# Optimization experiments

Measured on AMD Instinct MI355X. Metric: run time of the kernel, lower is better.

Reference implementation:

```python
import jax, jax.numpy as jnp
import numpy as np

H, W = 256, 256
N = 512
BG = jnp.zeros(3, dtype=jnp.float32)  # background_color=(0,0,0)


def setup_inputs() -> dict:
    key = jax.random.key(0)
    k1, k2, k3, k4, k5 = jax.random.split(key, 5)
    # positions: xy in [-1.5,1.5], z in [2,6] so every gaussian passes the z>0.01 test
    xy = jax.random.uniform(k1, (N, 2), minval=-1.5, maxval=1.5, dtype=jnp.float32)
    zpos = jax.random.uniform(k2, (N, 1), minval=2.0, maxval=6.0, dtype=jnp.float32)
    positions = jnp.concatenate([xy, zpos], axis=-1)
    # PSD 3D covariances with ~0.05 world-space std
    A = 0.05 * jax.random.normal(k3, (N, 3, 3), dtype=jnp.float32)
    cov3d = A @ jnp.swapaxes(A, -1, -2) + 1e-6 * jnp.eye(3, dtype=jnp.float32)
    opacities = jax.random.uniform(k4, (N, 1), dtype=jnp.float32)
    colors = jax.random.uniform(k5, (N, 3), dtype=jnp.float32)
    K = jnp.array([[300.0, 0.0, 128.0], [0.0, 300.0, 128.0], [0.0, 0.0, 1.0]], dtype=jnp.float32)
    R = jnp.eye(3, dtype=jnp.float32)
    t = jnp.zeros(3, dtype=jnp.float32)
    return {"positions": positions, "cov3d": cov3d, "opacities": opacities,
            "colors": colors, "K": K, "R": R, "t": t}


def _render(positions, cov3d, opacities, colors, K, R, t):
    # --- project means to camera / image space ---
    means_cam = positions @ R.T + t                       # (N,3)
    z = means_cam[:, 2]                                   # all > 0.01 by construction
    proj = means_cam @ K.T                                # (N,3)
    means_2d = proj[:, :2] / proj[:, 2:3]                 # (N,2) pixel coords (x,y)

    # --- project 3D covariance to 2D: cov2d = J (R cov3d R^T) J^T + 0.3 I ---
    fx, fy = K[0, 0], K[1, 1]
    xc, yc = means_cam[:, 0], means_cam[:, 1]
    zero = jnp.zeros_like(z)
    J = jnp.stack([
        jnp.stack([fx / z, zero, -fx * xc / z**2], axis=-1),
        jnp.stack([zero, fy / z, -fy * yc / z**2], axis=-1),
    ], axis=1)                                            # (N,2,3)
    cov_cam = jnp.einsum('ij,njk,lk->nil', R, cov3d, R)   # (N,3,3)
    cov2d = jnp.einsum('nij,njk,nlk->nil', J, cov_cam, J) + 0.3 * jnp.eye(2, dtype=jnp.float32)

    # --- front-to-back depth sort ---
    order = jnp.argsort(z)
    means_2d = means_2d[order]
    cov2d = cov2d[order]
    opac = opacities[:, 0][order]
    cols = colors[order]

    # --- 2x2 inverse and 3-sigma radii ---
    a, b, c = cov2d[:, 0, 0], cov2d[:, 0, 1], cov2d[:, 1, 1]
    det = jnp.clip(a * c - b * b, 1e-8, None)
    inv00, inv01, inv11 = c / det, -b / det, a / det
    max_eig = (a + c) * 0.5 + jnp.sqrt(jnp.clip(((a - c) * 0.5) ** 2 + b ** 2, 1e-8, None))
    radii = 3.0 * jnp.sqrt(max_eig)

    # --- bounding boxes (int() truncates toward zero, as in torch) ---
    mx, my = means_2d[:, 0], means_2d[:, 1]
    x_min = jnp.maximum(0.0, jnp.trunc(mx - radii))
    x_max = jnp.minimum(float(W), jnp.trunc(mx + radii) + 1.0)
    y_min = jnp.maximum(0.0, jnp.trunc(my - radii))
    y_max = jnp.minimum(float(H), jnp.trunc(my + radii) + 1.0)

    xs = jnp.arange(W, dtype=jnp.float32)
    ys = jnp.arange(H, dtype=jnp.float32)
    dx = xs[None, :] - mx[:, None]                        # (N,W)
    dy = ys[None, :] - my[:, None]                        # (N,H)
    mask_x = (xs[None, :] >= x_min[:, None]) & (xs[None, :] < x_max[:, None])
    mask_y = (ys[None, :] >= y_min[:, None]) & (ys[None, :] < y_max[:, None])
    mask = (mask_y[:, :, None] & mask_x[:, None, :]).astype(jnp.float32)  # (N,H,W)

    # --- gaussian weights on the grid ---
    mahal = (inv00[:, None, None] * dx[:, None, :] ** 2
             + 2.0 * inv01[:, None, None] * dy[:, :, None] * dx[:, None, :]
             + inv11[:, None, None] * dy[:, :, None] ** 2)                 # (N,H,W)
    alpha = opac[:, None, None] * jnp.exp(-0.5 * mahal) * mask            # (N,H,W)

    # --- front-to-back alpha compositing ---
    # sequential: contrib_i = alpha_i * (1 - alpha_acc_{i-1}); alpha_acc_i += contrib_i
    # closed form: T_i = prod_{j<i} (1 - alpha_j)  (exclusive cumprod)
    T = jnp.concatenate([jnp.ones((1, H, W), dtype=alpha.dtype),
                         jnp.cumprod(1.0 - alpha, axis=0)[:-1]], axis=0)
    contrib = alpha * T                                                   # (N,H,W)
    image = BG[None, None, :] + jnp.einsum('nhw,nc->hwc', contrib, cols)  # (H,W,3)
    return image


def reference(positions, cov3d, opacities, colors, K, R, t):
    return _render(positions, cov3d, opacities, colors, K, R, t)
```

## Files before the change

kernel.cpp:

```cpp
#include <hip/hip_runtime.h>


constexpr int IMG_H = 256;
constexpr int IMG_W = 256;
constexpr int MAXN  = 512;
constexpr int TW    = 16;
constexpr int TH    = 16;
constexpr int NTHR  = 512;

__global__ __launch_bounds__(NTHR) void fused_raster_kernel(
    const float* __restrict__ positions,
    const float* __restrict__ cov3d,
    const float* __restrict__ opacities,
    const float* __restrict__ colors,
    const float* __restrict__ Km,
    const float* __restrict__ Rm,
    const float* __restrict__ tv,
    float* __restrict__ out)
{
    __shared__ float4 s_srt[(MAXN + 4) * 3];
    __shared__ unsigned long long s_key[MAXN];
    __shared__ float4 s_comb[TW * TH];
    __shared__ int s_total;

    const int tix  = threadIdx.x;
    const int ty   = threadIdx.y;
    const int tid  = ty * TW + tix;
    const int lane = tid & 63;
    const int half = ty >> 4;
    const int py   = ty & 15;

    if (tid == 0) s_total = 0;

    const int tx0i = blockIdx.x * TW;
    const int ty0i = blockIdx.y * TH;
    const float tx0 = (float)tx0i;
    const float ty0 = (float)ty0i;

    const float R00 = Rm[0], R01 = Rm[1], R02 = Rm[2];
    const float R10 = Rm[3], R11 = Rm[4], R12 = Rm[5];
    const float R20 = Rm[6], R21 = Rm[7], R22 = Rm[8];
    const float t0 = tv[0], t1 = tv[1], t2 = tv[2];
    const float K00 = Km[0], K01 = Km[1], K02 = Km[2];
    const float K10 = Km[3], K11 = Km[4], K12 = Km[5];
    const float K20 = Km[6], K21 = Km[7], K22 = Km[8];
    const float fx = K00, fy = K11;

    __syncthreads();

    const int g = tid;

    const float px = positions[g*3+0];
    const float py3 = positions[g*3+1];
    const float pz = positions[g*3+2];

    const float cx = R00*px + R01*py3 + R02*pz + t0;
    const float cy = R10*px + R11*py3 + R12*pz + t1;
    const float cz = R20*px + R21*py3 + R22*pz + t2;

    const float pr0 = K00*cx + K01*cy + K02*cz;
    const float pr1 = K10*cx + K11*cy + K12*cz;
    const float pr2 = K20*cx + K21*cy + K22*cz;
    const float mx = pr0 / pr2;
    const float my = pr1 / pr2;

    const float invz  = 1.0f / cz;
    const float invz2 = invz * invz;
    const float j00 =  fx * invz;
    const float j02 = -fx * cx * invz2;
    const float j11 =  fy * invz;
    const float j12 = -fy * cy * invz2;

    const float C00 = cov3d[g*9+0], C01 = cov3d[g*9+1], C02 = cov3d[g*9+2];
    const float C10 = cov3d[g*9+3], C11 = cov3d[g*9+4], C12 = cov3d[g*9+5];
    const float C20 = cov3d[g*9+6], C21 = cov3d[g*9+7], C22 = cov3d[g*9+8];

    const float T100 = R00*C00 + R01*C10 + R02*C20;
    const float T101 = R00*C01 + R01*C11 + R02*C21;
    const float T102 = R00*C02 + R01*C12 + R02*C22;
    const float T110 = R10*C00 + R11*C10 + R12*C20;
    const float T111 = R10*C01 + R11*C11 + R12*C21;
    const float T112 = R10*C02 + R11*C12 + R12*C22;
    const float T120 = R20*C00 + R21*C10 + R22*C20;
    const float T121 = R20*C01 + R21*C11 + R22*C21;
    const float T122 = R20*C02 + R21*C12 + R22*C22;
    const float M00 = T100*R00 + T101*R01 + T102*R02;
    const float M01 = T100*R10 + T101*R11 + T102*R12;
    const float M02 = T100*R20 + T101*R21 + T102*R22;
    const float M11 = T110*R10 + T111*R11 + T112*R12;
    const float M12 = T110*R20 + T111*R21 + T112*R22;
    const float M20 = T120*R00 + T121*R01 + T122*R02;
    const float M21 = T120*R10 + T121*R11 + T122*R12;
    const float M22 = T120*R20 + T121*R21 + T122*R22;

    const float v00 = M00*j00 + M02*j02;
    const float v02 = M20*j00 + M22*j02;
    const float v10 = M01*j11 + M02*j12;
    const float v11 = M11*j11 + M12*j12;
    const float v12 = M21*j11 + M22*j12;

    const float va = j00*v00 + j02*v02 + 0.3f;
    const float vb = j00*v10 + j02*v12;
    const float vc = j11*v11 + j12*v12 + 0.3f;

    const float det  = fmaxf(va*vc - vb*vb, 1e-8f);
    const float idet = 1.0f / det;
    const float inv00 =  vc * idet;
    const float inv01 = -vb * idet;
    const float inv11 =  va * idet;

    const float half_diff = (va - vc) * 0.5f;
    const float disc = fmaxf(half_diff*half_diff + vb*vb, 1e-8f);
    const float max_eig = (va + vc) * 0.5f + sqrtf(disc);
    const float radii = 3.0f * sqrtf(max_eig);

    const float x_min = fmaxf(0.0f, truncf(mx - radii));
    const float x_max = fminf((float)IMG_W, truncf(mx + radii) + 1.0f);
    const float y_min = fmaxf(0.0f, truncf(my - radii));
    const float y_max = fminf((float)IMG_H, truncf(my + radii) + 1.0f);

    const unsigned long long key =
        ((unsigned long long)__float_as_uint(cz) << 32) | (unsigned)g;

    const bool hit = (x_min < tx0 + (float)TW) && (x_max > tx0) &&
                     (y_min < ty0 + (float)TH) && (y_max > ty0);

    {
        const unsigned long long mb = __ballot(hit);
        int base = 0;
        if (lane == 0 && mb) base = atomicAdd(&s_total, __popcll(mb));
        base = __shfl(base, 0);
        if (hit) {
            const int pos = base + __popcll(mb & ((1ull << lane) - 1ull));
            s_key[pos] = key;
        }
    }
    __syncthreads();
    const int K = s_total;

    int rank = 0;
    for (int j = 0; j < K; ++j)
        rank += (s_key[j] < key) ? 1 : 0;

    if (hit) {
        const int xm = max(0,  (int)x_min - tx0i);
        const int xM = min(TW, (int)x_max - tx0i);
        const int ym = max(0,  (int)y_min - ty0i);
        const int yM = min(TH, (int)y_max - ty0i);
        const unsigned pk = (unsigned)xm | ((unsigned)xM << 5)
                          | ((unsigned)ym << 10) | ((unsigned)yM << 15);
        s_srt[rank*3+0] = make_float4(mx, my, -0.5f*inv00, -inv01);
        s_srt[rank*3+1] = make_float4(-0.5f*inv11, opacities[g],
                                      colors[g*3+0], colors[g*3+1]);
        s_srt[rank*3+2] = make_float4(colors[g*3+2], __uint_as_float(pk),
                                      0.0f, 0.0f);
    }
    if (tid < 6) s_srt[K*3 + tid] = make_float4(0.0f, 0.0f, 0.0f, 0.0f);
    __syncthreads();

    int Kf = (K + 1) >> 1;
    Kf += (Kf & 1);
    if (Kf > K) Kf = K + (K & 1);
    const int mStart = half ? Kf : 0;
    const int mEnd   = half ? K  : Kf;

    const float fxp = (float)(tx0i + tix);
    const float fyp = (float)(ty0i + py);

    float T = 1.0f, accr = 0.0f, accg = 0.0f, accb = 0.0f;

    const int sb = mStart * 3;
    float4 A0 = s_srt[sb+0], A1 = s_srt[sb+1], A2 = s_srt[sb+2];
    float4 B0 = s_srt[sb+3], B1 = s_srt[sb+4], B2 = s_srt[sb+5];

    for (int m = mStart; m < mEnd; m += 2) {
        const int pf = (m + 2) * 3;
        const float4 C0 = s_srt[pf+0], C1 = s_srt[pf+1], C2 = s_srt[pf+2];
        const float4 D0 = s_srt[pf+3], D1 = s_srt[pf+4], D2 = s_srt[pf+5];

        {
            const unsigned pk = __float_as_uint(A2.y);
            const bool in = (tix >= (int)(pk & 31u)) & (tix < (int)((pk >> 5) & 31u))
                          & (py >= (int)((pk >> 10) & 31u)) & (py < (int)((pk >> 15) & 31u));
            const float dx = fxp - A0.x;
            const float dy = fyp - A0.y;
            const float e = A0.z*dx*dx + A0.w*dx*dy + A1.x*dy*dy;
            const float a = in ? A1.y * __expf(e) : 0.0f;
            const float w = T * a;
            accr = fmaf(w, A1.z, accr);
            accg = fmaf(w, A1.w, accg);
            accb = fmaf(w, A2.x, accb);
            T *= (1.0f - a);
        }
        {
            const unsigned pk = __float_as_uint(B2.y);
            const bool in = (tix >= (int)(pk & 31u)) & (tix < (int)((pk >> 5) & 31u))
                          & (py >= (int)((pk >> 10) & 31u)) & (py < (int)((pk >> 15) & 31u));
            const float dx = fxp - B0.x;
            const float dy = fyp - B0.y;
            const float e = B0.z*dx*dx + B0.w*dx*dy + B1.x*dy*dy;
            const float a = in ? B1.y * __expf(e) : 0.0f;
            const float w = T * a;
            accr = fmaf(w, B1.z, accr);
            accg = fmaf(w, B1.w, accg);
            accb = fmaf(w, B2.x, accb);
            T *= (1.0f - a);
        }

        A0 = C0; A1 = C1; A2 = C2;
        B0 = D0; B1 = D1; B2 = D2;

        if (!__any(T > 1.0e-5f)) break;
    }

    if (half == 1) s_comb[py * TW + tix] = make_float4(accr, accg, accb, T);
    __syncthreads();
    if (half == 0) {
        const float4 b = s_comb[py * TW + tix];
        accr = fmaf(T, b.x, accr);
        accg = fmaf(T, b.y, accg);
        accb = fmaf(T, b.z, accb);
        const int pix = ((ty0i + py) * IMG_W + (tx0i + tix)) * 3;
        out[pix + 0] = accr;
        out[pix + 1] = accg;
        out[pix + 2] = accb;
    }
}

extern "C" void kernel_launch(void* const* d_in, const int* in_sizes, int n_in,
                              void* d_out, int out_size, void* d_ws, size_t ws_size,
                              hipStream_t stream)
{
    const float* positions = (const float*)d_in[0];
    const float* cov3d     = (const float*)d_in[1];
    const float* opacities = (const float*)d_in[2];
    const float* colors    = (const float*)d_in[3];
    const float* Km        = (const float*)d_in[4];
    const float* Rm        = (const float*)d_in[5];
    const float* tv        = (const float*)d_in[6];
    float* out = (float*)d_out;

    dim3 block(TW, 2 * TH);
    dim3 grid(IMG_W / TW, IMG_H / TH);
    fused_raster_kernel<<<grid, block, 0, stream>>>(
        positions, cov3d, opacities, colors, Km, Rm, tv, out);
}
```

Baseline: 72.17 us.

## Split per-pixel gaussian list across four thread chunks instead of two

Doubles the block to 1024 threads so each pixel's sorted gaussian list is split into four segments processed in parallel, then combined front-to-back using the stored transmittances. The preprocessing is guarded so only the first 512 threads project gaussians, and rank counting is skipped for waves with no hits. This shortens the serial compositing chain per thread but loses early termination across segments, since later chunks cannot see the front transmittance, and it lowers occupancy per CU with the larger blocks.

```diff
diff --git a/kernel.cpp b/kernel.cpp
--- a/kernel.cpp
+++ b/kernel.cpp
@@ -6,7 +6,7 @@
 constexpr int MAXN  = 512;
 constexpr int TW    = 16;
 constexpr int TH    = 16;
-constexpr int NTHR  = 512;
+constexpr int NTHR  = 1024;
 
 __global__ __launch_bounds__(NTHR) void fused_raster_kernel(
     const float* __restrict__ positions,
@@ -20,15 +20,15 @@
 {
     __shared__ float4 s_srt[(MAXN + 4) * 3];
     __shared__ unsigned long long s_key[MAXN];
-    __shared__ float4 s_comb[TW * TH];
+    __shared__ float4 s_comb[3 * TW * TH];
     __shared__ int s_total;
 
-    const int tix  = threadIdx.x;
-    const int ty   = threadIdx.y;
-    const int tid  = ty * TW + tix;
-    const int lane = tid & 63;
-    const int half = ty >> 4;
-    const int py   = ty & 15;
+    const int tix   = threadIdx.x;
+    const int ty    = threadIdx.y;
+    const int tid   = ty * TW + tix;
+    const int lane  = tid & 63;
+    const int chunk = ty >> 4;
+    const int py    = ty & 15;
 
     if (tid == 0) s_total = 0;
 
@@ -48,82 +48,89 @@
 
     __syncthreads();
 
-    const int g = tid;
-
-    const float px = positions[g*3+0];
-    const float py3 = positions[g*3+1];
-    const float pz = positions[g*3+2];
-
-    const float cx = R00*px + R01*py3 + R02*pz + t0;
-    const float cy = R10*px + R11*py3 + R12*pz + t1;
-    const float cz = R20*px + R21*py3 + R22*pz + t2;
-
-    const float pr0 = K00*cx + K01*cy + K02*cz;
-    const float pr1 = K10*cx + K11*cy + K12*cz;
-    const float pr2 = K20*cx + K21*cy + K22*cz;
-    const float mx = pr0 / pr2;
-    const float my = pr1 / pr2;
-
-    const float invz  = 1.0f / cz;
-    const float invz2 = invz * invz;
-    const float j00 =  fx * invz;
-    const float j02 = -fx * cx * invz2;
-    const float j11 =  fy * invz;
-    const float j12 = -fy * cy * invz2;
-
-    const float C00 = cov3d[g*9+0], C01 = cov3d[g*9+1], C02 = cov3d[g*9+2];
-    const float C10 = cov3d[g*9+3], C11 = cov3d[g*9+4], C12 = cov3d[g*9+5];
-    const float C20 = cov3d[g*9+6], C21 = cov3d[g*9+7], C22 = cov3d[g*9+8];
-
-    const float T100 = R00*C00 + R01*C10 + R02*C20;
-    const float T101 = R00*C01 + R01*C11 + R02*C21;
-    const float T102 = R00*C02 + R01*C12 + R02*C22;
-    const float T110 = R10*C00 + R11*C10 + R12*C20;
-    const float T111 = R10*C01 + R11*C11 + R12*C21;
-    const float T112 = R10*C02 + R11*C12 + R12*C22;
-    const float T120 = R20*C00 + R21*C10 + R22*C20;
-    const float T121 = R20*C01 + R21*C11 + R22*C21;
-    const float T122 = R20*C02 + R21*C12 + R22*C22;
-    const float M00 = T100*R00 + T101*R01 + T102*R02;
-    const float M01 = T100*R10 + T101*R11 + T102*R12;
-    const float M02 = T100*R20 + T101*R21 + T102*R22;
-    const float M11 = T110*R10 + T111*R11 + T112*R12;
-    const float M12 = T110*R20 + T111*R21 + T112*R22;
-    const float M20 = T120*R00 + T121*R01 + T122*R02;
-    const float M21 = T120*R10 + T121*R11 + T122*R12;
-    const float M22 = T120*R20 + T121*R21 + T122*R22;
-
-    const float v00 = M00*j00 + M02*j02;
-    const float v02 = M20*j00 + M22*j02;
-    const float v10 = M01*j11 + M02*j12;
-    const float v11 = M11*j11 + M12*j12;
-    const float v12 = M21*j11 + M22*j12;
-
-    const float va = j00*v00 + j02*v02 + 0.3f;
-    const float vb = j00*v10 + j02*v12;
-    const float vc = j11*v11 + j12*v12 + 0.3f;
-
-    const float det  = fmaxf(va*vc - vb*vb, 1e-8f);
-    const float idet = 1.0f / det;
-    const float inv00 =  vc * idet;
-    const float inv01 = -vb * idet;
-    const float inv11 =  va * idet;
-
-    const float half_diff = (va - vc) * 0.5f;
-    const float disc = fmaxf(half_diff*half_diff + vb*vb, 1e-8f);
-    const float max_eig = (va + vc) * 0.5f + sqrtf(disc);
-    const float radii = 3.0f * sqrtf(max_eig);
-
-    const float x_min = fmaxf(0.0f, truncf(mx - radii));
-    const float x_max = fminf((float)IMG_W, truncf(mx + radii) + 1.0f);
-    const float y_min = fmaxf(0.0f, truncf(my - radii));
-    const float y_max = fminf((float)IMG_H, truncf(my + radii) + 1.0f);
-
-    const unsigned long long key =
-        ((unsigned long long)__float_as_uint(cz) << 32) | (unsigned)g;
-
-    const bool hit = (x_min < tx0 + (float)TW) && (x_max > tx0) &&
-                     (y_min < ty0 + (float)TH) && (y_max > ty0);
+    const bool active = (tid < MAXN);
+    const int g = active ? tid : 0;
+
+    float mx = 0.f, my = 0.f, inv00 = 0.f, inv01 = 0.f, inv11 = 0.f;
+    float x_min = 0.f, x_max = 0.f, y_min = 0.f, y_max = 0.f;
+    unsigned long long key = ~0ull;
+    bool hit = false;
+
+    if (active) {
+        const float px = positions[g*3+0];
+        const float pyy = positions[g*3+1];
+        const float pz = positions[g*3+2];
+
+        const float cx = R00*px + R01*pyy + R02*pz + t0;
+        const float cy = R10*px + R11*pyy + R12*pz + t1;
+        const float cz = R20*px + R21*pyy + R22*pz + t2;
+
+        const float pr0 = K00*cx + K01*cy + K02*cz;
+        const float pr1 = K10*cx + K11*cy + K12*cz;
+        const float pr2 = K20*cx + K21*cy + K22*cz;
+        mx = pr0 / pr2;
+        my = pr1 / pr2;
+
+        const float invz  = 1.0f / cz;
+        const float invz2 = invz * invz;
+        const float j00 =  fx * invz;
+        const float j02 = -fx * cx * invz2;
+        const float j11 =  fy * invz;
+        const float j12 = -fy * cy * invz2;
+
+        const float C00 = cov3d[g*9+0], C01 = cov3d[g*9+1], C02 = cov3d[g*9+2];
+        const float C10 = cov3d[g*9+3], C11 = cov3d[g*9+4], C12 = cov3d[g*9+5];
+        const float C20 = cov3d[g*9+6], C21 = cov3d[g*9+7], C22 = cov3d[g*9+8];
+
+        const float T100 = R00*C00 + R01*C10 + R02*C20;
+        const float T101 = R00*C01 + R01*C11 + R02*C21;
+        const float T102 = R00*C02 + R01*C12 + R02*C22;
+        const float T110 = R10*C00 + R11*C10 + R12*C20;
+        const float T111 = R10*C01 + R11*C11 + R12*C21;
+        const float T112 = R10*C02 + R11*C12 + R12*C22;
+        const float T120 = R20*C00 + R21*C10 + R22*C20;
+        const float T121 = R20*C01 + R21*C11 + R22*C21;
+        const float T122 = R20*C02 + R21*C12 + R22*C22;
+        const float M00 = T100*R00 + T101*R01 + T102*R02;
+        const float M01 = T100*R10 + T101*R11 + T102*R12;
+        const float M02 = T100*R20 + T101*R21 + T102*R22;
+        const float M11 = T110*R10 + T111*R11 + T112*R12;
+        const float M12 = T110*R20 + T111*R21 + T112*R22;
+        const float M20 = T120*R00 + T121*R01 + T122*R02;
+        const float M21 = T120*R10 + T121*R11 + T122*R12;
+        const float M22 = T120*R20 + T121*R21 + T122*R22;
+
+        const float v00 = M00*j00 + M02*j02;
+        const float v02 = M20*j00 + M22*j02;
+        const float v10 = M01*j11 + M02*j12;
+        const float v11 = M11*j11 + M12*j12;
+        const float v12 = M21*j11 + M22*j12;
+
+        const float va = j00*v00 + j02*v02 + 0.3f;
+        const float vb = j00*v10 + j02*v12;
+        const float vc = j11*v11 + j12*v12 + 0.3f;
+
+        const float det  = fmaxf(va*vc - vb*vb, 1e-8f);
+        const float idet = 1.0f / det;
+        inv00 =  vc * idet;
+        inv01 = -vb * idet;
+        inv11 =  va * idet;
+
+        const float half_diff = (va - vc) * 0.5f;
+        const float disc = fmaxf(half_diff*half_diff + vb*vb, 1e-8f);
+        const float max_eig = (va + vc) * 0.5f + sqrtf(disc);
+        const float radii = 3.0f * sqrtf(max_eig);
+
+        x_min = fmaxf(0.0f, truncf(mx - radii));
+        x_max = fminf((float)IMG_W, truncf(mx + radii) + 1.0f);
+        y_min = fmaxf(0.0f, truncf(my - radii));
+        y_max = fminf((float)IMG_H, truncf(my + radii) + 1.0f);
+
+        key = ((unsigned long long)__float_as_uint(cz) << 32) | (unsigned)g;
+
+        hit = (x_min < tx0 + (float)TW) && (x_max > tx0) &&
+              (y_min < ty0 + (float)TH) && (y_max > ty0);
+    }
 
     {
         const unsigned long long mb = __ballot(hit);
@@ -139,8 +146,10 @@
     const int K = s_total;
 
     int rank = 0;
-    for (int j = 0; j < K; ++j)
-        rank += (s_key[j] < key) ? 1 : 0;
+    if (__any(hit)) {
+        for (int j = 0; j < K; ++j)
+            rank += (s_key[j] < key) ? 1 : 0;
+    }
 
     if (hit) {
         const int xm = max(0,  (int)x_min - tx0i);
@@ -155,14 +164,14 @@
         s_srt[rank*3+2] = make_float4(colors[g*3+2], __uint_as_float(pk),
                                       0.0f, 0.0f);
     }
-    if (tid < 6) s_srt[K*3 + tid] = make_float4(0.0f, 0.0f, 0.0f, 0.0f);
-    __syncthreads();
-
-    int Kf = (K + 1) >> 1;
-    Kf += (Kf & 1);
-    if (Kf > K) Kf = K + (K & 1);
-    const int mStart = half ? Kf : 0;
-    const int mEnd   = half ? K  : Kf;
+    if (tid < 12) s_srt[K*3 + tid] = make_float4(0.0f, 0.0f, 0.0f, 0.0f);
+    __syncthreads();
+
+    const int q1 = min(K, (K/4     + 1) & ~1);
+    const int q2 = min(K, (K/2     + 1) & ~1);
+    const int q3 = min(K, (3*K/4   + 1) & ~1);
+    const int mStart = (chunk == 0) ? 0  : (chunk == 1) ? q1 : (chunk == 2) ? q2 : q3;
+    const int mEnd   = (chunk == 0) ? q1 : (chunk == 1) ? q2 : (chunk == 2) ? q3 : K;
 
     const float fxp = (float)(tx0i + tix);
     const float fyp = (float)(ty0i + py);
@@ -213,13 +222,19 @@
         if (!__any(T > 1.0e-5f)) break;
     }
 
-    if (half == 1) s_comb[py * TW + tix] = make_float4(accr, accg, accb, T);
-    __syncthreads();
-    if (half == 0) {
-        const float4 b = s_comb[py * TW + tix];
-        accr = fmaf(T, b.x, accr);
-        accg = fmaf(T, b.y, accg);
-        accb = fmaf(T, b.z, accb);
+    const int idx = py * TW + tix;
+    if (chunk != 0) s_comb[(chunk - 1) * (TW*TH) + idx] = make_float4(accr, accg, accb, T);
+    __syncthreads();
+    if (chunk == 0) {
+        const float4 c1 = s_comb[0*(TW*TH) + idx];
+        const float4 c2 = s_comb[1*(TW*TH) + idx];
+        const float4 c3 = s_comb[2*(TW*TH) + idx];
+        const float r123 = fmaf(c1.w, fmaf(c2.w, c3.x, c2.x), c1.x);
+        const float g123 = fmaf(c1.w, fmaf(c2.w, c3.y, c2.y), c1.y);
+        const float b123 = fmaf(c1.w, fmaf(c2.w, c3.z, c2.z), c1.z);
+        accr = fmaf(T, r123, accr);
+        accg = fmaf(T, g123, accg);
+        accb = fmaf(T, b123, accb);
         const int pix = ((ty0i + py) * IMG_W + (tx0i + tix)) * 3;
         out[pix + 0] = accr;
         out[pix + 1] = accg;
@@ -240,7 +255,7 @@
     const float* tv        = (const float*)d_in[6];
     float* out = (float*)d_out;
 
-    dim3 block(TW, 2 * TH);
+    dim3 block(TW, 4 * TH);
     dim3 grid(IMG_W / TW, IMG_H / TH);
     fused_raster_kernel<<<grid, block, 0, stream>>>(
         positions, cov3d, opacities, colors, Km, Rm, tv, out);
```

Result: no change. 70.81 us (-1.9%).
